# Kernel tuning notes

Hardware: AMD Instinct MI355X
Metric: run time of the kernel (lower is better)

The kernel has to match this reference:

```python
import jax, jax.numpy as jnp
import numpy as np

B, S, HID = 2, 2048, 2048
HEADS, KV_HEADS = 16, 4
HD = HID // HEADS  # 128
KV_DIM = KV_HEADS * HD  # 512


def apply_rope(x, cos, sin):
    # x: [..., S, D]; cos/sin: [S, D//2] broadcast over leading dims
    even, odd = x[..., 0::2], x[..., 1::2]
    out = jnp.stack((even * cos - odd * sin, even * sin + odd * cos), axis=-1)
    return out.reshape(x.shape)


def setup_inputs() -> dict:
    key = jax.random.key(0)
    ks = jax.random.split(key, 6)
    x = jax.random.normal(ks[0], (B, S, HID), dtype=jnp.float32)
    # realistic RoPE tables
    inv_freq = 1.0 / (10000.0 ** (np.arange(0, HD, 2, dtype=np.float32) / HD))  # [HD/2]
    ang = np.arange(S, dtype=np.float32)[:, None] * inv_freq[None, :]           # [S, HD/2]
    cos = jnp.asarray(np.cos(ang))
    sin = jnp.asarray(np.sin(ang))
    std = 0.02
    Wq = jax.random.normal(ks[1], (HID, HID), dtype=jnp.float32) * std   # [out, in]
    Wk = jax.random.normal(ks[2], (KV_DIM, HID), dtype=jnp.float32) * std
    Wv = jax.random.normal(ks[3], (KV_DIM, HID), dtype=jnp.float32) * std
    Wo = jax.random.normal(ks[4], (HID, HID), dtype=jnp.float32) * std
    return {"x": x, "cos": cos, "sin": sin, "Wq": Wq, "Wk": Wk, "Wv": Wv, "Wo": Wo}


def reference(x, cos, sin, Wq, Wk, Wv, Wo):
    batch, seq, _ = x.shape
    q = jnp.einsum('bsi,oi->bso', x, Wq).reshape(batch, seq, HEADS, HD).transpose(0, 2, 1, 3)
    k = jnp.einsum('bsi,oi->bso', x, Wk).reshape(batch, seq, KV_HEADS, HD).transpose(0, 2, 1, 3)
    v = jnp.einsum('bsi,oi->bso', x, Wv).reshape(batch, seq, KV_HEADS, HD).transpose(0, 2, 1, 3)
    q = apply_rope(q, cos, sin)
    k = apply_rope(k, cos, sin)
    repeats = HEADS // KV_HEADS
    k = jnp.repeat(k, repeats, axis=1)  # [B, H, S, D]
    v = jnp.repeat(v, repeats, axis=1)
    scale = 1.0 / jnp.sqrt(jnp.asarray(HD, dtype=q.dtype))
    scores = jnp.einsum('bhqd,bhkd->bhqk', q, k) * scale
    causal = jnp.tril(jnp.ones((seq, seq), dtype=bool))
    scores = jnp.where(causal, scores, jnp.finfo(scores.dtype).min)
    attn = jax.nn.softmax(scores, axis=-1)
    y = jnp.einsum('bhqk,bhkd->bhqd', attn, v)
    y = y.transpose(0, 2, 1, 3).reshape(batch, seq, HID)
    return jnp.einsum('bso,io->bsi', y, Wo.T) if False else jnp.einsum('bsi,oi->bso', y, Wo)
```

## Files before the change

kernel.cpp:

```cpp
#include <hip/hip_runtime.h>

using u16 = unsigned short;
using u32 = unsigned int;

typedef __bf16 bf16x8 __attribute__((ext_vector_type(8)));
typedef float f32x4 __attribute__((ext_vector_type(4)));

#define MFMA16(a, b, c) __builtin_amdgcn_mfma_f32_16x16x32_bf16(a, b, c, 0, 0, 0)

__device__ __forceinline__ u16 f2bf(float f) {
    u32 u = __builtin_bit_cast(u32, f);
    u = (u + 0x7fffu + ((u >> 16) & 1u)) >> 16;
    return (u16)u;
}
__device__ __forceinline__ float bf2f(u16 h) {
    u32 u = ((u32)h) << 16;
    return __builtin_bit_cast(float, u);
}

__device__ __forceinline__ float fexp2(float x) {
#if __has_builtin(__builtin_amdgcn_exp2f)
    return __builtin_amdgcn_exp2f(x);
#else
    return exp2f(x);
#endif
}

__device__ __forceinline__ void async_ld16(const u16* g, u16* l) {
    __builtin_amdgcn_global_load_lds(
        (const __attribute__((address_space(1))) void*)g,
        (__attribute__((address_space(3))) void*)l,
        16, 0, 0);
}

__global__ void cast_all(const float* __restrict__ x, const float* __restrict__ wq,
                         const float* __restrict__ wk, const float* __restrict__ wv,
                         const float* __restrict__ wo, u16* __restrict__ dst) {
    int i = blockIdx.x * 256 + threadIdx.x;
    const float* src; int off;
    if (i < 2097152)      { src = x;  off = 0; }
    else if (i < 3145728) { src = wq; off = 2097152; }
    else if (i < 3407872) { src = wk; off = 3145728; }
    else if (i < 3670016) { src = wv; off = 3407872; }
    else                  { src = wo; off = 3670016; }
    float4 f = ((const float4*)src)[i - off];
    ushort4 u;
    u.x = f2bf(f.x); u.y = f2bf(f.y); u.z = f2bf(f.z); u.w = f2bf(f.w);
    ((ushort4*)dst)[i] = u;
}

template <int MODE>
__global__ __launch_bounds__(256, 2) void gemm_bt(
    const u16* __restrict__ A, const u16* __restrict__ Bw,
    void* __restrict__ C0, u16* __restrict__ Ck, u16* __restrict__ Cv, int N, int K)
{
    __shared__ __align__(16) u16 ldsA[8192];
    __shared__ __align__(16) u16 ldsB[8192];
    const int tid = threadIdx.x;
    const int w = tid >> 6, lane = tid & 63;
    const int lm = lane & 15, g = lane >> 4, lk = g << 3;
    const int m0 = blockIdx.y * 128, n0 = blockIdx.x * 128;
    const int wm = (w >> 1) * 64, wn = (w & 1) * 64;

    f32x4 acc[4][4] = {};

    for (int k0 = 0; k0 < K; k0 += 64) {
        __syncthreads();
#pragma unroll
        for (int i = 0; i < 4; ++i) {
            const int bk = i * 4 + w;
            const int mt = bk >> 1, kt = bk & 1;
            async_ld16(A + (size_t)(m0 + mt * 16 + lm) * K + k0 + kt * 32 + lk, &ldsA[bk * 512]);
            async_ld16(Bw + (size_t)(n0 + mt * 16 + lm) * K + k0 + kt * 32 + lk, &ldsB[bk * 512]);
        }
        __syncthreads();
#pragma unroll
        for (int kt = 0; kt < 2; ++kt) {
            bf16x8 af[4], bfr[4];
#pragma unroll
            for (int i = 0; i < 4; ++i) {
                af[i] = *(const bf16x8*)&ldsA[((wm >> 4) + i) * 1024 + kt * 512 + lane * 8];
                bfr[i] = *(const bf16x8*)&ldsB[((wn >> 4) + i) * 1024 + kt * 512 + lane * 8];
            }
#pragma unroll
            for (int mi = 0; mi < 4; ++mi)
#pragma unroll
                for (int ni = 0; ni < 4; ++ni)
                    acc[mi][ni] = MFMA16(af[mi], bfr[ni], acc[mi][ni]);
        }
    }

    const bool odd = lane & 1;
#pragma unroll
    for (int mi = 0; mi < 4; ++mi) {
#pragma unroll
        for (int ni = 0; ni < 4; ++ni) {
            const int row0 = m0 + wm + mi * 16 + g * 4;
            const int c = n0 + wn + ni * 16 + lm;
            if constexpr (MODE == 2) {
#pragma unroll
                for (int r = 0; r < 4; ++r) {
                    float v = acc[mi][ni][r];
                    float pv = __shfl_xor(v, 1);
                    if (!odd) {
                        float2 st2; st2.x = v; st2.y = pv;
                        *(float2*)((float*)C0 + (size_t)(row0 + r) * N + c) = st2;
                    }
                }
            } else {
                if (n0 >= 2560) {
                    const int cv = c - 2560;
                    const int bb = row0 >> 11, s = row0 & 2047;
                    ushort4 pk;
                    pk.x = f2bf(acc[mi][ni][0]); pk.y = f2bf(acc[mi][ni][1]);
                    pk.z = f2bf(acc[mi][ni][2]); pk.w = f2bf(acc[mi][ni][3]);
                    *(ushort4*)(Cv + ((size_t)(bb * 512 + cv) << 11) + s) = pk;
                } else {
                    const bool isQ = (n0 < 2048);
                    const int cc = isQ ? c : c - 2048;
                    const int ld = isQ ? 2048 : 512;
                    u16* dst = isQ ? (u16*)C0 : Ck;
#pragma unroll
                    for (int r = 0; r < 4; ++r) {
                        float v = acc[mi][ni][r];
                        float pv = __shfl_xor(v, 1);
                        if (!odd) {
                            ushort2 st2; st2.x = f2bf(v); st2.y = f2bf(pv);
                            *(ushort2*)(dst + (size_t)(row0 + r) * ld + cc) = st2;
                        }
                    }
                }
            }
        }
    }
}

__global__ void rope_kernel(u16* __restrict__ Qw, u16* __restrict__ Kw,
                            const float* __restrict__ cosT, const float* __restrict__ sinT) {
    int tid = blockIdx.x * 256 + threadIdx.x;
    const int QP = 4096 * 1024;
    u16* base; int row, colp, ld;
    if (tid < QP) { base = Qw; row = tid >> 10; colp = tid & 1023; ld = 2048; }
    else { int t = tid - QP; base = Kw; row = t >> 8; colp = t & 255; ld = 512; }
    const int j = colp & 63, s = row & 2047;
    u16* p = base + (size_t)row * ld + colp * 2;
    ushort2 qp = *(ushort2*)p;
    const float e = bf2f(qp.x), o = bf2f(qp.y);
    const float c = cosT[s * 64 + j], sn = sinT[s * 64 + j];
    ushort2 r2; r2.x = f2bf(e * c - o * sn); r2.y = f2bf(e * sn + o * c);
    *(ushort2*)p = r2;
}

__global__ __launch_bounds__(256, 3) void attn_fwd(
    const u16* __restrict__ Q, const u16* __restrict__ Kk,
    const u16* __restrict__ Vt, u16* __restrict__ Y)
{
    __shared__ __align__(16) u16 ldsK[8192];
    __shared__ __align__(16) u16 ldsV[8192];
    __shared__ __align__(16) u16 ldsP[4 * 32 * 72];
    const int tid = threadIdx.x;
    const int w = tid >> 6, lane = tid & 63;
    const int lm = lane & 15, g = lane >> 4, lk = g << 3;
    const int qt = 15 - (blockIdx.x >> 5);
    const int bh = blockIdx.x & 31;
    const int b = bh >> 4, h = bh & 15, kvh = h >> 2;
    const int q0 = qt * 128;
    const float C1 = 0.08838834764831845f * 1.44269504088896341f;
    const float C2 = 12.0f * 1.44269504088896341f;

    bf16x8 qf[2][4];
#pragma unroll
    for (int st = 0; st < 2; ++st)
#pragma unroll
        for (int kt = 0; kt < 4; ++kt)
            qf[st][kt] = *(const bf16x8*)(Q + (size_t)(b * 2048 + q0 + w * 32 + st * 16 + lm) * 2048
                                          + h * 128 + kt * 32 + lk);

    float lsum[2][4] = {};
    f32x4 oacc[2][8] = {};

    const int ktiles = qt * 2 + 2;
    for (int t = 0; t < ktiles; ++t) {
        const bool masked = (t >= ktiles - 2);
        const int k0 = t * 64;
        __syncthreads();
#pragma unroll
        for (int i = 0; i < 4; ++i) {
            const int bk = i * 4 + w;
            {
                const int nt = bk >> 2, kt = bk & 3;
                async_ld16(Kk + (size_t)(b * 2048 + k0 + nt * 16 + lm) * 512 + kvh * 128 + kt * 32 + lk,
                           &ldsK[bk * 512]);
            }
            {
                const int nt = bk >> 1, kt = bk & 1;
                async_ld16(Vt + (size_t)(b * 512 + kvh * 128 + nt * 16 + lm) * 2048 + k0 + kt * 32 + lk,
                           &ldsV[bk * 512]);
            }
        }
        __syncthreads();

        f32x4 sacc[2][4] = {};
#pragma unroll
        for (int nt = 0; nt < 4; ++nt)
#pragma unroll
            for (int kt = 0; kt < 4; ++kt) {
                bf16x8 bf = *(const bf16x8*)&ldsK[(nt * 4 + kt) * 512 + lane * 8];
                sacc[0][nt] = MFMA16(qf[0][kt], bf, sacc[0][nt]);
                sacc[1][nt] = MFMA16(qf[1][kt], bf, sacc[1][nt]);
            }

#pragma unroll
        for (int st = 0; st < 2; ++st)
#pragma unroll
            for (int nt = 0; nt < 4; ++nt)
#pragma unroll
                for (int r = 0; r < 4; ++r) {
                    float p = fexp2(fmaf(sacc[st][nt][r], C1, -C2));
                    if (masked) {
                        const int key = k0 + nt * 16 + lm;
                        const int qr = q0 + w * 32 + st * 16 + g * 4 + r;
                        p = (key > qr) ? 0.f : p;
                    }
                    sacc[st][nt][r] = p;
                    lsum[st][r] += p;
                }

#pragma unroll
        for (int st = 0; st < 2; ++st)
#pragma unroll
            for (int nt = 0; nt < 4; ++nt)
#pragma unroll
                for (int r = 0; r < 4; ++r)
                    ldsP[w * 2304 + (st * 16 + g * 4 + r) * 72 + nt * 16 + lm] = f2bf(sacc[st][nt][r]);
        asm volatile("s_waitcnt lgkmcnt(0)" ::: "memory");

#pragma unroll
        for (int kt = 0; kt < 2; ++kt) {
            bf16x8 af0 = *(const bf16x8*)&ldsP[w * 2304 + lm * 72 + kt * 32 + lk];
            bf16x8 af1 = *(const bf16x8*)&ldsP[w * 2304 + (16 + lm) * 72 + kt * 32 + lk];
#pragma unroll
            for (int n8 = 0; n8 < 8; ++n8) {
                bf16x8 bf = *(const bf16x8*)&ldsV[(n8 * 2 + kt) * 512 + lane * 8];
                oacc[0][n8] = MFMA16(af0, bf, oacc[0][n8]);
                oacc[1][n8] = MFMA16(af1, bf, oacc[1][n8]);
            }
        }
    }

#pragma unroll
    for (int st = 0; st < 2; ++st)
#pragma unroll
        for (int r = 0; r < 4; ++r) {
#pragma unroll
            for (int d = 1; d < 16; d <<= 1) lsum[st][r] += __shfl_xor(lsum[st][r], d);
            const float inv = 1.f / lsum[st][r];
            const int row = b * 2048 + q0 + w * 32 + st * 16 + g * 4 + r;
#pragma unroll
            for (int n8 = 0; n8 < 8; ++n8) {
                float v = oacc[st][n8][r] * inv;
                float pv = __shfl_xor(v, 1);
                if (!(lane & 1)) {
                    ushort2 o2; o2.x = f2bf(v); o2.y = f2bf(pv);
                    *(ushort2*)(Y + (size_t)row * 2048 + h * 128 + n8 * 16 + lm) = o2;
                }
            }
        }
}

extern "C" void kernel_launch(void* const* d_in, const int* in_sizes, int n_in,
                              void* d_out, int out_size, void* d_ws, size_t ws_size,
                              hipStream_t stream) {
    const float* x    = (const float*)d_in[0];
    const float* cosT = (const float*)d_in[1];
    const float* sinT = (const float*)d_in[2];
    const float* Wq   = (const float*)d_in[3];
    const float* Wk   = (const float*)d_in[4];
    const float* Wv   = (const float*)d_in[5];
    const float* Wo   = (const float*)d_in[6];

    u16* ws    = (u16*)d_ws;
    u16* xb    = ws;
    u16* Wqkvb = xb + 8388608;
    u16* Wob   = Wqkvb + 6291456;
    u16* Qws   = Wob + 4194304;
    u16* Kws   = Qws + 8388608;
    u16* Vtws  = Kws + 2097152;
    u16* Yws   = Vtws + 2097152;
    if (ws_size < (size_t)39845888 * 2) return;

    dim3 blk(256);
    cast_all<<<18432, blk, 0, stream>>>(x, Wq, Wk, Wv, Wo, ws);
    gemm_bt<3><<<dim3(24, 32), blk, 0, stream>>>(xb, Wqkvb, (void*)Qws, Kws, Vtws, 3072, 2048);
    rope_kernel<<<20480, blk, 0, stream>>>(Qws, Kws, cosT, sinT);
    attn_fwd<<<512, blk, 0, stream>>>(Qws, Kws, Vtws, Yws);
    gemm_bt<2><<<dim3(16, 32), blk, 0, stream>>>(Yws, Wob, d_out, nullptr, nullptr, 2048, 2048);
}
```

Before: 451.5 us.

## Double-buffer K/V tiles in attention and halve the query tile to 64 rows

The attention kernel now keeps two LDS buffers for K and V and issues the async loads for the next key tile before computing on the current one, so global loads overlap the MFMA work. The query tile per block shrinks from 128 to 64 rows (16 per wave), which doubles the grid to 1024 blocks and makes only the last tile need causal masking. The cost is double the K/V LDS footprint, occupancy bounds lowered from 3 to 2, and each K/V tile loaded from LDS serving half as many query rows. There is also a single __syncthreads per iteration and no visible wait on the async loads before the next tile is consumed, which may rely on the async_ld16 semantics.

```diff
diff --git a/kernel.cpp b/kernel.cpp
--- a/kernel.cpp
+++ b/kernel.cpp
@@ -151,121 +151,130 @@
     *(ushort2*)p = r2;
 }
 
-__global__ __launch_bounds__(256, 3) void attn_fwd(
+__global__ __launch_bounds__(256, 2) void attn_fwd(
     const u16* __restrict__ Q, const u16* __restrict__ Kk,
     const u16* __restrict__ Vt, u16* __restrict__ Y)
 {
-    __shared__ __align__(16) u16 ldsK[8192];
-    __shared__ __align__(16) u16 ldsV[8192];
-    __shared__ __align__(16) u16 ldsP[4 * 32 * 72];
+    __shared__ __align__(16) u16 ldsK[2][8192];
+    __shared__ __align__(16) u16 ldsV[2][8192];
+    __shared__ __align__(16) u16 ldsP[4][1152];
     const int tid = threadIdx.x;
     const int w = tid >> 6, lane = tid & 63;
     const int lm = lane & 15, g = lane >> 4, lk = g << 3;
-    const int qt = 15 - (blockIdx.x >> 5);
+    const int qt = 31 - (blockIdx.x >> 5);
     const int bh = blockIdx.x & 31;
     const int b = bh >> 4, h = bh & 15, kvh = h >> 2;
-    const int q0 = qt * 128;
+    const int q0 = qt * 64;
     const float C1 = 0.08838834764831845f * 1.44269504088896341f;
     const float C2 = 12.0f * 1.44269504088896341f;
 
-    bf16x8 qf[2][4];
-#pragma unroll
-    for (int st = 0; st < 2; ++st)
-#pragma unroll
-        for (int kt = 0; kt < 4; ++kt)
-            qf[st][kt] = *(const bf16x8*)(Q + (size_t)(b * 2048 + q0 + w * 32 + st * 16 + lm) * 2048
-                                          + h * 128 + kt * 32 + lk);
-
-    float lsum[2][4] = {};
-    f32x4 oacc[2][8] = {};
-
-    const int ktiles = qt * 2 + 2;
+    bf16x8 qf[4];
+#pragma unroll
+    for (int kt = 0; kt < 4; ++kt)
+        qf[kt] = *(const bf16x8*)(Q + (size_t)(b * 2048 + q0 + w * 16 + lm) * 2048
+                                  + h * 128 + kt * 32 + lk);
+
+    float lsum[4] = {};
+    f32x4 oacc[8] = {};
+
+    const int ktiles = qt + 1;
+
+#pragma unroll
+    for (int i = 0; i < 4; ++i) {
+        const int bk = i * 4 + w;
+        {
+            const int nt = bk >> 2, kt = bk & 3;
+            async_ld16(Kk + (size_t)(b * 2048 + nt * 16 + lm) * 512 + kvh * 128 + kt * 32 + lk,
+                       &ldsK[0][bk * 512]);
+        }
+        {
+            const int nt = bk >> 1, kt = bk & 1;
+            async_ld16(Vt + (size_t)(b * 512 + kvh * 128 + nt * 16 + lm) * 2048 + kt * 32 + lk,
+                       &ldsV[0][bk * 512]);
+        }
+    }
+
     for (int t = 0; t < ktiles; ++t) {
-        const bool masked = (t >= ktiles - 2);
+        const int cur = t & 1;
         const int k0 = t * 64;
         __syncthreads();
-#pragma unroll
-        for (int i = 0; i < 4; ++i) {
-            const int bk = i * 4 + w;
-            {
-                const int nt = bk >> 2, kt = bk & 3;
-                async_ld16(Kk + (size_t)(b * 2048 + k0 + nt * 16 + lm) * 512 + kvh * 128 + kt * 32 + lk,
-                           &ldsK[bk * 512]);
-            }
-            {
-                const int nt = bk >> 1, kt = bk & 1;
-                async_ld16(Vt + (size_t)(b * 512 + kvh * 128 + nt * 16 + lm) * 2048 + k0 + kt * 32 + lk,
-                           &ldsV[bk * 512]);
-            }
-        }
-        __syncthreads();
-
-        f32x4 sacc[2][4] = {};
+
+        if (t + 1 < ktiles) {
+            const int nk0 = k0 + 64, nb = cur ^ 1;
+#pragma unroll
+            for (int i = 0; i < 4; ++i) {
+                const int bk = i * 4 + w;
+                {
+                    const int nt = bk >> 2, kt = bk & 3;
+                    async_ld16(Kk + (size_t)(b * 2048 + nk0 + nt * 16 + lm) * 512 + kvh * 128 + kt * 32 + lk,
+                               &ldsK[nb][bk * 512]);
+                }
+                {
+                    const int nt = bk >> 1, kt = bk & 1;
+                    async_ld16(Vt + (size_t)(b * 512 + kvh * 128 + nt * 16 + lm) * 2048 + nk0 + kt * 32 + lk,
+                               &ldsV[nb][bk * 512]);
+                }
+            }
+        }
+
+        f32x4 sacc[4] = {};
 #pragma unroll
         for (int nt = 0; nt < 4; ++nt)
 #pragma unroll
             for (int kt = 0; kt < 4; ++kt) {
-                bf16x8 bf = *(const bf16x8*)&ldsK[(nt * 4 + kt) * 512 + lane * 8];
-                sacc[0][nt] = MFMA16(qf[0][kt], bf, sacc[0][nt]);
-                sacc[1][nt] = MFMA16(qf[1][kt], bf, sacc[1][nt]);
-            }
-
-#pragma unroll
-        for (int st = 0; st < 2; ++st)
-#pragma unroll
-            for (int nt = 0; nt < 4; ++nt)
-#pragma unroll
-                for (int r = 0; r < 4; ++r) {
-                    float p = fexp2(fmaf(sacc[st][nt][r], C1, -C2));
-                    if (masked) {
-                        const int key = k0 + nt * 16 + lm;
-                        const int qr = q0 + w * 32 + st * 16 + g * 4 + r;
-                        p = (key > qr) ? 0.f : p;
-                    }
-                    sacc[st][nt][r] = p;
-                    lsum[st][r] += p;
-                }
-
-#pragma unroll
-        for (int st = 0; st < 2; ++st)
-#pragma unroll
-            for (int nt = 0; nt < 4; ++nt)
-#pragma unroll
-                for (int r = 0; r < 4; ++r)
-                    ldsP[w * 2304 + (st * 16 + g * 4 + r) * 72 + nt * 16 + lm] = f2bf(sacc[st][nt][r]);
+                bf16x8 bf = *(const bf16x8*)&ldsK[cur][(nt * 4 + kt) * 512 + lane * 8];
+                sacc[nt] = MFMA16(qf[kt], bf, sacc[nt]);
+            }
+
+        const bool masked = (t == ktiles - 1);
+#pragma unroll
+        for (int nt = 0; nt < 4; ++nt)
+#pragma unroll
+            for (int r = 0; r < 4; ++r) {
+                float p = fexp2(fmaf(sacc[nt][r], C1, -C2));
+                if (masked) {
+                    const int key = k0 + nt * 16 + lm;
+                    const int qr = q0 + w * 16 + g * 4 + r;
+                    p = (key > qr) ? 0.f : p;
+                }
+                sacc[nt][r] = p;
+                lsum[r] += p;
+            }
+
+#pragma unroll
+        for (int nt = 0; nt < 4; ++nt)
+#pragma unroll
+            for (int r = 0; r < 4; ++r)
+                ldsP[w][(g * 4 + r) * 72 + nt * 16 + lm] = f2bf(sacc[nt][r]);
         asm volatile("s_waitcnt lgkmcnt(0)" ::: "memory");
 
 #pragma unroll
         for (int kt = 0; kt < 2; ++kt) {
-            bf16x8 af0 = *(const bf16x8*)&ldsP[w * 2304 + lm * 72 + kt * 32 + lk];
-            bf16x8 af1 = *(const bf16x8*)&ldsP[w * 2304 + (16 + lm) * 72 + kt * 32 + lk];
+            bf16x8 af = *(const bf16x8*)&ldsP[w][lm * 72 + kt * 32 + lk];
 #pragma unroll
             for (int n8 = 0; n8 < 8; ++n8) {
-                bf16x8 bf = *(const bf16x8*)&ldsV[(n8 * 2 + kt) * 512 + lane * 8];
-                oacc[0][n8] = MFMA16(af0, bf, oacc[0][n8]);
-                oacc[1][n8] = MFMA16(af1, bf, oacc[1][n8]);
-            }
-        }
-    }
-
-#pragma unroll
-    for (int st = 0; st < 2; ++st)
-#pragma unroll
-        for (int r = 0; r < 4; ++r) {
-#pragma unroll
-            for (int d = 1; d < 16; d <<= 1) lsum[st][r] += __shfl_xor(lsum[st][r], d);
-            const float inv = 1.f / lsum[st][r];
-            const int row = b * 2048 + q0 + w * 32 + st * 16 + g * 4 + r;
-#pragma unroll
-            for (int n8 = 0; n8 < 8; ++n8) {
-                float v = oacc[st][n8][r] * inv;
-                float pv = __shfl_xor(v, 1);
-                if (!(lane & 1)) {
-                    ushort2 o2; o2.x = f2bf(v); o2.y = f2bf(pv);
-                    *(ushort2*)(Y + (size_t)row * 2048 + h * 128 + n8 * 16 + lm) = o2;
-                }
-            }
-        }
+                bf16x8 bf = *(const bf16x8*)&ldsV[cur][(n8 * 2 + kt) * 512 + lane * 8];
+                oacc[n8] = MFMA16(af, bf, oacc[n8]);
+            }
+        }
+    }
+
+#pragma unroll
+    for (int r = 0; r < 4; ++r) {
+#pragma unroll
+        for (int d = 1; d < 16; d <<= 1) lsum[r] += __shfl_xor(lsum[r], d);
+        const float inv = 1.f / lsum[r];
+        const int row = b * 2048 + q0 + w * 16 + g * 4 + r;
+#pragma unroll
+        for (int n8 = 0; n8 < 8; ++n8) {
+            float v = oacc[n8][r] * inv;
+            float pv = __shfl_xor(v, 1);
+            if (!(lane & 1)) {
+                ushort2 o2; o2.x = f2bf(v); o2.y = f2bf(pv);
+                *(ushort2*)(Y + (size_t)row * 2048 + h * 128 + n8 * 16 + lm) = o2;
+            }
+        }
+    }
 }
 
 extern "C" void kernel_launch(void* const* d_in, const int* in_sizes, int n_in,
@@ -293,6 +302,6 @@
     cast_all<<<18432, blk, 0, stream>>>(x, Wq, Wk, Wv, Wo, ws);
     gemm_bt<3><<<dim3(24, 32), blk, 0, stream>>>(xb, Wqkvb, (void*)Qws, Kws, Vtws, 3072, 2048);
     rope_kernel<<<20480, blk, 0, stream>>>(Qws, Kws, cosT, sinT);
-    attn_fwd<<<512, blk, 0, stream>>>(Qws, Kws, Vtws, Yws);
+    attn_fwd<<<1024, blk, 0, stream>>>(Qws, Kws, Vtws, Yws);
     gemm_bt<2><<<dim3(16, 32), blk, 0, stream>>>(Yws, Wob, d_out, nullptr, nullptr, 2048, 2048);
 }
```

Measured after the change: 375.5 us. -16.8%, faster.
